# Kernel optimization log

Hardware: AMD Instinct MI355X
Metric: run time of the kernel (lower is better)

Reference implementation:

```python
import jax, jax.numpy as jnp
import numpy as np

DIM = 512
NT = 4      # n_tapes
HD = 64     # head_dim (mem_size)
SEQ = 1024
BATCH = 32
EPS = 1e-12


def _unitnorm(v, axis=-1):
    n = jnp.linalg.norm(v, axis=axis, keepdims=True)
    return v / jnp.maximum(n, EPS)


def setup_inputs() -> dict:
    key = jax.random.key(0)
    ks = jax.random.split(key, 16)
    s = 0.02
    p = lambda k, shape: jax.random.normal(k, shape, jnp.float32) * s
    return {
        "inputs": jax.random.normal(ks[0], (SEQ, BATCH, DIM), jnp.float32),
        "W_ih": p(ks[1], (4 * DIM, DIM)),
        "W_hh": p(ks[2], (4 * DIM, DIM)),
        "b_ih": p(ks[3], (4 * DIM,)),
        "b_hh": p(ks[4], (4 * DIM,)),
        "W_act": p(ks[5], (6 * NT, DIM)),
        "b_act": p(ks[6], (6 * NT,)),
        "W_val": p(ks[7], (HD * NT, DIM)),
        "b_val": p(ks[8], (HD * NT,)),
        "W_key": p(ks[9], (HD * NT, DIM)),
        "b_key": p(ks[10], (HD * NT,)),
        "W_q": p(ks[11], (HD * NT, DIM)),
        "b_q": p(ks[12], (HD * NT,)),
        "W_out": p(ks[13], (DIM, HD * NT)),
        "b_out": p(ks[14], (DIM,)),
        "tapelen": 64,
    }


def _lstm(inputs, W_ih, W_hh, b_ih, b_hh):
    # torch nn.LSTM, single layer, unidirectional, zero init state.
    S, B, D = inputs.shape
    gx = inputs @ W_ih.T + (b_ih + b_hh)  # [S,B,4D]

    def step(carry, g):
        h, c = carry
        g = g + h @ W_hh.T
        i, f, gg, o = jnp.split(g, 4, axis=-1)  # torch gate order i,f,g,o
        c = jax.nn.sigmoid(f) * c + jax.nn.sigmoid(i) * jnp.tanh(gg)
        h = jax.nn.sigmoid(o) * jnp.tanh(c)
        return (h, c), h

    h0 = jnp.zeros((B, D), inputs.dtype)
    (_, _), hs = jax.lax.scan(step, (h0, h0), gx)
    return hs  # [S,B,D]


def reference(inputs, W_ih, W_hh, b_ih, b_hh, W_act, b_act, W_val, b_val,
              W_key, b_key, W_q, b_q, W_out, b_out, tapelen):
    S, B, D = inputs.shape
    values = (inputs @ W_val.T + b_val).reshape(S, B, NT, HD)
    keys = _unitnorm((inputs @ W_key.T + b_key).reshape(S, B, NT, HD))

    hidden = _lstm(inputs, W_ih, W_hh, b_ih, b_hh)
    actions = (hidden @ W_act.T + b_act).reshape(S, B, NT, 6)
    dir_r = jax.nn.softmax(actions[..., 0:2], axis=-1)   # [S,B,NT,2]
    dir_w = jax.nn.softmax(actions[..., 2:4], axis=-1)
    rwprobs = jax.nn.sigmoid(actions[..., 4:6])
    queries = _unitnorm((hidden @ W_q.T + b_q).reshape(S, B, NT, HD))

    tape0 = jnp.zeros((tapelen, B, NT, HD), inputs.dtype)
    tkey0 = jnp.zeros_like(tape0)
    pos0 = jnp.zeros((tapelen, B, NT), inputs.dtype).at[0].set(1.0)

    def step(carry, xs):
        tape, tape_key, rpos, wpos = carry
        v, k, q, rd, wd, rw = xs
        wprob = rw[None, :, :, 1:2]                       # write gate
        oldval = jnp.einsum('lntc,lnt->ntc', tape, wpos)
        tape = tape + wpos[..., None] * (v - oldval)[None] * wprob
        read_out = jnp.einsum('lntc,lnt->ntc', tape, rpos)
        oldkey = jnp.einsum('lntc,lnt->ntc', tape_key, wpos)
        tape_key = tape_key + wpos[..., None] * (k - oldkey)[None] * wprob
        jpos = jnp.einsum('lntc,ntc->lnt', tape_key, q)
        jn = jnp.linalg.norm(jpos, axis=0, keepdims=True)  # normalize over tapelen
        jpos = jpos / jnp.maximum(jn, EPS)
        wpos_n = wpos * wd[None, :, :, 0] + jpos * wd[None, :, :, 1]
        out = read_out * rw[:, :, 0:1]                     # read gate
        rpos_n = rpos * rd[None, :, :, 0] + jpos * rd[None, :, :, 1]
        return (tape, tape_key, rpos_n, wpos_n), out

    (tape, _, _, _), read_outs = jax.lax.scan(
        step, (tape0, tkey0, pos0, pos0),
        (values, keys, queries, dir_r, dir_w, rwprobs))

    outputs = read_outs.reshape(S, B, NT * HD) @ W_out.T + b_out
    return outputs, tape.reshape(tapelen, B, HD * NT)
```

## Files before the change

### kernel.cpp

```cpp
#include <hip/hip_runtime.h>

typedef short short8 __attribute__((ext_vector_type(8)));
typedef float f32x4 __attribute__((ext_vector_type(4)));

__device__ __forceinline__ unsigned short f2bf(float x) {
  unsigned u = __builtin_bit_cast(unsigned, x);
  u += 0x7fffu + ((u >> 16) & 1u);
  return (unsigned short)(u >> 16);
}
__device__ __forceinline__ float bf2f(unsigned short v) {
  return __builtin_bit_cast(float, (unsigned)v << 16);
}
__device__ __forceinline__ float sigf(float x) { return 1.f / (1.f + __expf(-x)); }

__device__ __forceinline__ void split8(const float* __restrict__ vv, short8* h8, short8* l8) {
#pragma unroll
  for (int j = 0; j < 8; j++) {
    unsigned short hb = f2bf(vv[j]);
    unsigned short lb = f2bf(vv[j] - bf2f(hb));
    (*h8)[j] = (short)hb; (*l8)[j] = (short)lb;
  }
}
__device__ __forceinline__ void split_store8(const float* __restrict__ src,
                                             unsigned short* __restrict__ dhi,
                                             unsigned short* __restrict__ dlo) {
  float4 v0 = *(const float4*)src, v1 = *(const float4*)(src + 4);
  float vv[8] = {v0.x, v0.y, v0.z, v0.w, v1.x, v1.y, v1.z, v1.w};
  short8 h8, l8;
  split8(vv, &h8, &l8);
  *(short8*)dhi = h8; *(short8*)dlo = l8;
}

static constexpr size_t OFF_GX    = 0;
static constexpr size_t OFF_HC    = OFF_GX   + (size_t)4096*2048*4;
static constexpr size_t OFF_QUER  = OFF_HC   + (size_t)4096*512*4;
static constexpr size_t OFF_ACTS  = OFF_QUER + (size_t)32768*256*4;
static constexpr size_t OFF_R     = OFF_ACTS + (size_t)32768*24*4;
static constexpr size_t OFF_HB16  = OFF_R    + (size_t)32768*256*4;
static constexpr size_t OFF_CBUF  = OFF_HB16 + (size_t)2*2*32*512*2;
static constexpr size_t OFF_FLAGS = OFF_CBUF + (size_t)32*512*4;
static constexpr size_t WS_NEED   = OFF_FLAGS + 4096;

__global__ void zero_flags_kernel(unsigned int* flags) { flags[threadIdx.x] = 0u; }
__global__ void sentinel_kernel(float* p) { p[0] = 12345.0f; }

__global__ __launch_bounds__(256) void gemm_f32bt_kernel(
    const float* __restrict__ A, const float* __restrict__ Bw, float* __restrict__ C,
    const float* __restrict__ bias1, const float* __restrict__ bias2,
    int M, int N, int K) {
  const int bn = blockIdx.x, bm = blockIdx.y;
  const int tid = threadIdx.x;
  const int w = tid >> 6, l = tid & 63;
  const int wm = w >> 1, wn = w & 1;
  __shared__ __align__(16) unsigned short Ahs[128 * 40], Als[128 * 40];
  __shared__ __align__(16) unsigned short Bhs[128 * 40], Bls[128 * 40];
  f32x4 acc[4][4];
#pragma unroll
  for (int m = 0; m < 4; m++)
#pragma unroll
    for (int n = 0; n < 4; n++) acc[m][n] = (f32x4){0.f, 0.f, 0.f, 0.f};

  const int sr = tid >> 2;
  const int sk = (tid & 3) * 8;
  const size_t arow0 = (size_t)(bm * 128 + sr) * K;
  const size_t brow0 = (size_t)(bn * 128 + sr) * K;
  const int fr = l & 15, kb = (l >> 4) * 8;

  for (int kt = 0; kt < K; kt += 32) {
    __syncthreads();
    split_store8(A + arow0 + kt + sk,                  &Ahs[sr * 40 + sk],        &Als[sr * 40 + sk]);
    split_store8(A + arow0 + (size_t)64 * K + kt + sk, &Ahs[(sr + 64) * 40 + sk], &Als[(sr + 64) * 40 + sk]);
    split_store8(Bw + brow0 + kt + sk,                  &Bhs[sr * 40 + sk],        &Bls[sr * 40 + sk]);
    split_store8(Bw + brow0 + (size_t)64 * K + kt + sk, &Bhs[(sr + 64) * 40 + sk], &Bls[(sr + 64) * 40 + sk]);
    __syncthreads();
    short8 ah[4], al[4], bh[4], bl[4];
#pragma unroll
    for (int m = 0; m < 4; m++) {
      ah[m] = *(const short8*)&Ahs[(wm * 64 + m * 16 + fr) * 40 + kb];
      al[m] = *(const short8*)&Als[(wm * 64 + m * 16 + fr) * 40 + kb];
    }
#pragma unroll
    for (int n = 0; n < 4; n++) {
      bh[n] = *(const short8*)&Bhs[(wn * 64 + n * 16 + fr) * 40 + kb];
      bl[n] = *(const short8*)&Bls[(wn * 64 + n * 16 + fr) * 40 + kb];
    }
#pragma unroll
    for (int m = 0; m < 4; m++)
#pragma unroll
      for (int n = 0; n < 4; n++) {
        acc[m][n] = __builtin_amdgcn_mfma_f32_16x16x32_bf16(ah[m], bh[n], acc[m][n], 0, 0, 0);
        acc[m][n] = __builtin_amdgcn_mfma_f32_16x16x32_bf16(ah[m], bl[n], acc[m][n], 0, 0, 0);
        acc[m][n] = __builtin_amdgcn_mfma_f32_16x16x32_bf16(al[m], bh[n], acc[m][n], 0, 0, 0);
      }
  }
  const int cr = (l >> 4) * 4, cc = l & 15;
#pragma unroll
  for (int m = 0; m < 4; m++) {
#pragma unroll
    for (int n = 0; n < 4; n++) {
      int row0 = bm * 128 + wm * 64 + m * 16 + cr;
      int col = bn * 128 + wn * 64 + n * 16 + cc;
      float bv = bias1 ? bias1[col] : 0.f;
      if (bias2) bv += bias2[col];
#pragma unroll
      for (int r = 0; r < 4; r++) C[(size_t)(row0 + r) * N + col] = acc[m][n][r] + bv;
    }
  }
}

__global__ __launch_bounds__(256) void norm64_kernel(float* __restrict__ buf) {
  int g = blockIdx.x * 4 + (threadIdx.x >> 6);
  int lane = threadIdx.x & 63;
  float x = buf[(size_t)g * 64 + lane];
  float s = x * x;
#pragma unroll
  for (int m = 1; m < 64; m <<= 1) s += __shfl_xor(s, m, 64);
  buf[(size_t)g * 64 + lane] = x / fmaxf(sqrtf(s), 1e-12f);
}

__global__ __launch_bounds__(256) void lstm_kernel(const float* __restrict__ gxc,
                                                   const float* __restrict__ Whh,
                                                   unsigned short* __restrict__ hb16,
                                                   float* __restrict__ cbuf,
                                                   unsigned int* __restrict__ flags,
                                                   float* __restrict__ Hc,
                                                   int t0) {
  const int g = blockIdx.x;
  const int u0 = g * 8;
  const int tid = threadIdx.x;
  const int l = tid & 63, w = tid >> 6;
  __shared__ __align__(16) unsigned short Whi[32 * 512], Wlo[32 * 512];
  __shared__ __align__(16) unsigned short hhi[32 * 512], hlo[32 * 512];
  __shared__ float gates[32][33];

  {
    int r = tid >> 3, seg = tid & 7;
    int grow = (r >> 3) * 512 + u0 + (r & 7);
    const float* src = Whh + (size_t)grow * 512 + seg * 64;
#pragma unroll
    for (int i0 = 0; i0 < 64; i0 += 8) {
      int kg = seg * 8 + (i0 >> 3);
      int phys = r * 512 + ((kg ^ (r & 7)) << 3);
      split_store8(src + i0, &Whi[phys], &Wlo[phys]);
    }
  }
  if (t0 == 0) {
    for (int i = tid * 8; i < 32 * 512; i += 256 * 8) {
      short8 z = {0, 0, 0, 0, 0, 0, 0, 0};
      *(short8*)&hhi[i] = z; *(short8*)&hlo[i] = z;
    }
  }
  const int bb = tid >> 3, jj = tid & 7;
  float c = (t0 == 0) ? 0.f : cbuf[bb * 512 + u0 + jj];
  const int m = w >> 1, n = w & 1;
  const int arow = m * 16 + (l & 15), brow = n * 16 + (l & 15);
  const int asw = arow & 7, bsw = brow & 7;
  const int kq = l >> 4;
  __syncthreads();

  for (int t = t0; t < t0 + 128; ++t) {
    const float* gxr = gxc + ((size_t)(t - t0) * 32 + bb) * 2048;
    float xgi = gxr[u0 + jj];
    float xgf = gxr[512 + u0 + jj];
    float xgg = gxr[1024 + u0 + jj];
    float xgo = gxr[1536 + u0 + jj];
    if (t > 0) {
      if (tid < 64) {
        while (__hip_atomic_load(&flags[tid], __ATOMIC_RELAXED, __HIP_MEMORY_SCOPE_AGENT) < (unsigned)t)
          __builtin_amdgcn_s_sleep(1);
      }
      __syncthreads();
      const size_t pbase = (size_t)(t & 1) * 2 * 16384;
      const unsigned long long* hbh = (const unsigned long long*)(hb16 + pbase);
      const unsigned long long* hbl = (const unsigned long long*)(hb16 + pbase + 16384);
#pragma unroll
      for (int g8 = 0; g8 < 8; g8++) {
        int idx = g8 * 2048 + tid * 8;
        unsigned long long h0 = __hip_atomic_load(hbh + (idx >> 2),     __ATOMIC_RELAXED, __HIP_MEMORY_SCOPE_AGENT);
        unsigned long long h1 = __hip_atomic_load(hbh + (idx >> 2) + 1, __ATOMIC_RELAXED, __HIP_MEMORY_SCOPE_AGENT);
        unsigned long long l0 = __hip_atomic_load(hbl + (idx >> 2),     __ATOMIC_RELAXED, __HIP_MEMORY_SCOPE_AGENT);
        unsigned long long l1 = __hip_atomic_load(hbl + (idx >> 2) + 1, __ATOMIC_RELAXED, __HIP_MEMORY_SCOPE_AGENT);
        int b = idx >> 9, kg = (idx >> 3) & 63;
        int phys = b * 512 + ((kg ^ (b & 7)) << 3);
        *(unsigned long long*)&hhi[phys] = h0; *(unsigned long long*)&hhi[phys + 4] = h1;
        *(unsigned long long*)&hlo[phys] = l0; *(unsigned long long*)&hlo[phys + 4] = l1;
      }
      __syncthreads();
    }
    f32x4 acc = (f32x4){0.f, 0.f, 0.f, 0.f};
#pragma unroll
    for (int kt = 0; kt < 16; kt++) {
      int kg = kt * 4 + kq;
      short8 ah = *(const short8*)&hhi[arow * 512 + ((kg ^ asw) << 3)];
      short8 al = *(const short8*)&hlo[arow * 512 + ((kg ^ asw) << 3)];
      short8 bh = *(const short8*)&Whi[brow * 512 + ((kg ^ bsw) << 3)];
      short8 bl = *(const short8*)&Wlo[brow * 512 + ((kg ^ bsw) << 3)];
      acc = __builtin_amdgcn_mfma_f32_16x16x32_bf16(ah, bh, acc, 0, 0, 0);
      acc = __builtin_amdgcn_mfma_f32_16x16x32_bf16(ah, bl, acc, 0, 0, 0);
      acc = __builtin_amdgcn_mfma_f32_16x16x32_bf16(al, bh, acc, 0, 0, 0);
    }
    {
      int jcol = n * 16 + (l & 15), i0r = m * 16 + (l >> 4) * 4;
#pragma unroll
      for (int r = 0; r < 4; r++) gates[jcol][i0r + r] = acc[r];
    }
    __syncthreads();
    {
      float gi = gates[jj][bb]      + xgi;
      float gf = gates[8 + jj][bb]  + xgf;
      float gg = gates[16 + jj][bb] + xgg;
      float go = gates[24 + jj][bb] + xgo;
      c = sigf(gf) * c + sigf(gi) * tanhf(gg);
      float h = sigf(go) * tanhf(c);
      Hc[((size_t)(t - t0) * 32 + bb) * 512 + u0 + jj] = h;
      unsigned short hi16 = f2bf(h);
      unsigned short lo16 = f2bf(h - bf2f(hi16));
      const size_t pb2 = (size_t)((t + 1) & 1) * 2 * 16384;
      __hip_atomic_store(hb16 + pb2 + bb * 512 + u0 + jj, hi16,
                         __ATOMIC_RELAXED, __HIP_MEMORY_SCOPE_AGENT);
      __hip_atomic_store(hb16 + pb2 + 16384 + bb * 512 + u0 + jj, lo16,
                         __ATOMIC_RELAXED, __HIP_MEMORY_SCOPE_AGENT);
    }
    __syncthreads();
    if (tid == 0)
      __hip_atomic_store(&flags[g], (unsigned)(t + 1), __ATOMIC_RELAXED, __HIP_MEMORY_SCOPE_AGENT);
  }
  cbuf[bb * 512 + u0 + jj] = c;
}

__global__ __launch_bounds__(256) void actions_kernel(const float* __restrict__ H,
                                                      const float* __restrict__ Wact,
                                                      const float* __restrict__ bact,
                                                      float* __restrict__ acts) {
  const int wrow = threadIdx.x >> 6;
  const int row = blockIdx.x * 4 + wrow;
  const int lane = threadIdx.x & 63;
  __shared__ float a_s[4][24];
  const float* hp = H + (size_t)row * 512 + lane * 8;
  float4 h0 = *(const float4*)hp, h1 = *(const float4*)(hp + 4);
  float hf[8] = {h0.x, h0.y, h0.z, h0.w, h1.x, h1.y, h1.z, h1.w};
#pragma unroll
  for (int j = 0; j < 24; j++) {
    const float4* wr = (const float4*)(Wact + (size_t)j * 512 + lane * 8);
    float4 w0 = wr[0], w1 = wr[1];
    float p = hf[0] * w0.x + hf[1] * w0.y + hf[2] * w0.z + hf[3] * w0.w +
              hf[4] * w1.x + hf[5] * w1.y + hf[6] * w1.z + hf[7] * w1.w;
#pragma unroll
    for (int mm = 1; mm < 64; mm <<= 1) p += __shfl_xor(p, mm, 64);
    if (lane == j) a_s[wrow][j] = p + bact[j];
  }
  __syncthreads();
  if (lane < 4) {
    float av[6];
#pragma unroll
    for (int i = 0; i < 6; i++) av[i] = a_s[wrow][lane * 6 + i];
    float* o = acts + (size_t)row * 24 + lane * 6;
    o[0] = sigf(av[0] - av[1]); o[1] = sigf(av[1] - av[0]);
    o[2] = sigf(av[2] - av[3]); o[3] = sigf(av[3] - av[2]);
    o[4] = sigf(av[4]); o[5] = sigf(av[5]);
  }
}

__global__ __launch_bounds__(256) void tape_kernel(const float* __restrict__ vals,
                                                   const float* __restrict__ keys,
                                                   const float* __restrict__ quer,
                                                   const float* __restrict__ acts,
                                                   float* __restrict__ Rout,
                                                   float* __restrict__ out_tape) {
  const int bid = blockIdx.x;
  const int b = bid >> 2, nt = bid & 3;
  const int tid = threadIdx.x;
  const int cid = tid & 63, lg = tid >> 6;
  __shared__ float tape[64][65], tkey[64][65];
  __shared__ float redA[4][64], redB[4][64];
  __shared__ float wpos_s[64], rpos_s[64], q_s[64], dv_s[64], dk_s[64];
  for (int i = tid; i < 64 * 65; i += 256) { ((float*)tape)[i] = 0.f; ((float*)tkey)[i] = 0.f; }
  if (tid < 64) { wpos_s[tid] = (tid == 0) ? 1.f : 0.f; rpos_s[tid] = (tid == 0) ? 1.f : 0.f; }
  __syncthreads();

  float pv = 0.f, pk = 0.f, pq = 0.f;
  float2 pa0, pa1, pa2;
  {
    const size_t rc0 = ((size_t)b * 4 + nt) * 64;
    const float* a60 = acts + (size_t)b * 24 + nt * 6;
    if (tid < 64) { pv = vals[rc0 + tid]; pk = keys[rc0 + tid]; pq = quer[rc0 + tid]; }
    pa0 = *(const float2*)(a60); pa1 = *(const float2*)(a60 + 2); pa2 = *(const float2*)(a60 + 4);
  }

  for (int t = 0; t < 1024; ++t) {
    const float v = pv, k = pk, qv = pq;
    const float rd0 = pa0.x, rd1 = pa0.y, wd0 = pa1.x, wd1 = pa1.y, rw0 = pa2.x, rw1 = pa2.y;
    const size_t rc = (((size_t)t * 32 + b) * 4 + nt) * 64;
    if (tid < 64) q_s[tid] = qv;
    {
      int tn = (t + 1 < 1024) ? t + 1 : 1023;
      const size_t rbn = (size_t)tn * 32 + b;
      const size_t rcn = (rbn * 4 + nt) * 64;
      const float* a6n = acts + rbn * 24 + nt * 6;
      if (tid < 64) { pv = vals[rcn + tid]; pk = keys[rcn + tid]; pq = quer[rcn + tid]; }
      pa0 = *(const float2*)(a6n); pa1 = *(const float2*)(a6n + 2); pa2 = *(const float2*)(a6n + 4);
    }
    __syncthreads();
    float pa = 0.f, pb = 0.f;
#pragma unroll
    for (int i = 0; i < 16; i++) {
      int l2 = lg * 16 + i; float ww = wpos_s[l2];
      pa += tape[l2][cid] * ww; pb += tkey[l2][cid] * ww;
    }
    redA[lg][cid] = pa; redB[lg][cid] = pb;
    __syncthreads();
    if (tid < 64) {
      float ov = redA[0][cid] + redA[1][cid] + redA[2][cid] + redA[3][cid];
      float ok = redB[0][cid] + redB[1][cid] + redB[2][cid] + redB[3][cid];
      dv_s[cid] = (v - ov) * rw1;
      dk_s[cid] = (k - ok) * rw1;
    }
    __syncthreads();
    const float dv = dv_s[cid], dk = dk_s[cid];
    float pr = 0.f;
#pragma unroll
    for (int i = 0; i < 16; i++) {
      int l2 = lg * 16 + i; float ww = wpos_s[l2], r = rpos_s[l2];
      float tn2 = tape[l2][cid] + ww * dv; tape[l2][cid] = tn2; pr += tn2 * r;
      float kn = tkey[l2][cid] + ww * dk; tkey[l2][cid] = kn;
    }
    redA[lg][cid] = pr;
    __syncthreads();
    {
      const int lr = cid, cg = lg;
      float pj = 0.f;
#pragma unroll
      for (int i = 0; i < 16; i++) { int c2 = cg * 16 + i; pj += tkey[lr][c2] * q_s[c2]; }
      redB[cg][lr] = pj;
    }
    __syncthreads();
    if (tid < 64) {
      float jp = redB[0][tid] + redB[1][tid] + redB[2][tid] + redB[3][tid];
      float s = jp * jp;
#pragma unroll
      for (int mm = 1; mm < 64; mm <<= 1) s += __shfl_xor(s, mm, 64);
      jp /= fmaxf(sqrtf(s), 1e-12f);
      rpos_s[tid] = rpos_s[tid] * rd0 + jp * rd1;
      wpos_s[tid] = wpos_s[tid] * wd0 + jp * wd1;
    } else if (tid < 128) {
      int c2 = tid - 64;
      float ro = redA[0][c2] + redA[1][c2] + redA[2][c2] + redA[3][c2];
      Rout[rc + c2] = ro * rw0;
    }
  }
  __syncthreads();
  for (int i = tid; i < 4096; i += 256) {
    int l2 = i >> 6, c2 = i & 63;
    out_tape[((size_t)l2 * 32 + b) * 256 + nt * 64 + c2] = tape[l2][c2];
  }
}

extern "C" void kernel_launch(void* const* d_in, const int* in_sizes, int n_in,
                              void* d_out, int out_size, void* d_ws, size_t ws_size,
                              hipStream_t stream) {
  const float* inputs = (const float*)d_in[0];
  const float* W_ih = (const float*)d_in[1];
  const float* W_hh = (const float*)d_in[2];
  const float* b_ih = (const float*)d_in[3];
  const float* b_hh = (const float*)d_in[4];
  const float* W_act = (const float*)d_in[5];
  const float* b_act = (const float*)d_in[6];
  const float* W_val = (const float*)d_in[7];
  const float* b_val = (const float*)d_in[8];
  const float* W_key = (const float*)d_in[9];
  const float* b_key = (const float*)d_in[10];
  const float* W_q = (const float*)d_in[11];
  const float* b_q = (const float*)d_in[12];
  const float* W_out = (const float*)d_in[13];
  const float* b_out = (const float*)d_in[14];

  if (ws_size < WS_NEED) {
    sentinel_kernel<<<1, 1, 0, stream>>>((float*)d_out);
    return;
  }

  char* ws = (char*)d_ws;
  float* gxbuf = (float*)(ws + OFF_GX);
  float* Hc = (float*)(ws + OFF_HC);
  float* quer = (float*)(ws + OFF_QUER);
  float* acts = (float*)(ws + OFF_ACTS);
  float* R = (float*)(ws + OFF_R);
  unsigned short* hb16 = (unsigned short*)(ws + OFF_HB16);
  float* cbuf = (float*)(ws + OFF_CBUF);
  unsigned int* flags = (unsigned int*)(ws + OFF_FLAGS);

  float* keys = (float*)d_out;
  float* vals = (float*)d_out + 8388608;
  float* out_tape = (float*)d_out + 16777216;

  dim3 blk(256);
  zero_flags_kernel<<<1, 64, 0, stream>>>(flags);

  gemm_f32bt_kernel<<<dim3(2, 256), blk, 0, stream>>>(inputs, W_val, vals, b_val, nullptr, 32768, 256, 512);
  gemm_f32bt_kernel<<<dim3(2, 256), blk, 0, stream>>>(inputs, W_key, keys, b_key, nullptr, 32768, 256, 512);
  norm64_kernel<<<32768, blk, 0, stream>>>(keys);

  for (int q = 0; q < 8; q++) {
    const float* Achunk = inputs + (size_t)q * 4096 * 512;
    gemm_f32bt_kernel<<<dim3(16, 32), blk, 0, stream>>>(Achunk, W_ih, gxbuf, b_ih, b_hh, 4096, 2048, 512);
    lstm_kernel<<<64, blk, 0, stream>>>(gxbuf, W_hh, hb16, cbuf, flags, Hc, q * 128);
    gemm_f32bt_kernel<<<dim3(2, 32), blk, 0, stream>>>(Hc, W_q, quer + (size_t)q * 4096 * 256, b_q, nullptr, 4096, 256, 512);
    actions_kernel<<<1024, blk, 0, stream>>>(Hc, W_act, b_act, acts + (size_t)q * 4096 * 24);
  }
  norm64_kernel<<<32768, blk, 0, stream>>>(quer);

  tape_kernel<<<128, blk, 0, stream>>>(vals, keys, quer, acts, R, out_tape);

  gemm_f32bt_kernel<<<dim3(4, 256), blk, 0, stream>>>(R, W_out, (float*)d_out, b_out, nullptr, 32768, 512, 256);
}
```

Measured before the change: 7.878 ms.

## Use single-wave register-resident tape kernel and packed hi/lo LSTM hidden exchange

The tape recurrence kernel now runs one 64-thread wavefront per (batch, tape), keeping each column of the tape and the key tape in registers. All block barriers are dropped and only small LDS arrays are used for the position weights and the key-query products, which cuts per-step synchronisation on the 1024-step serial scan. The LSTM kernel packs the bf16 hi and lo halves of h into one 32-bit word, so each step needs one store per element and fewer, wider loads. Every wave now polls the flags with __all instead of one wave followed by a barrier. The costs are heavy register use (128 floats per thread) and more spinning across waves.

Result: slower. 12.51 ms (+58.8%).

```diff
diff --git a/kernel.cpp b/kernel.cpp
--- a/kernel.cpp
+++ b/kernel.cpp
@@ -36,8 +36,8 @@
 static constexpr size_t OFF_QUER  = OFF_HC   + (size_t)4096*512*4;
 static constexpr size_t OFF_ACTS  = OFF_QUER + (size_t)32768*256*4;
 static constexpr size_t OFF_R     = OFF_ACTS + (size_t)32768*24*4;
-static constexpr size_t OFF_HB16  = OFF_R    + (size_t)32768*256*4;
-static constexpr size_t OFF_CBUF  = OFF_HB16 + (size_t)2*2*32*512*2;
+static constexpr size_t OFF_HPK   = OFF_R    + (size_t)32768*256*4;
+static constexpr size_t OFF_CBUF  = OFF_HPK  + (size_t)2*32*512*4;
 static constexpr size_t OFF_FLAGS = OFF_CBUF + (size_t)32*512*4;
 static constexpr size_t WS_NEED   = OFF_FLAGS + 4096;
 
@@ -120,7 +120,7 @@
 
 __global__ __launch_bounds__(256) void lstm_kernel(const float* __restrict__ gxc,
                                                    const float* __restrict__ Whh,
-                                                   unsigned short* __restrict__ hb16,
+                                                   unsigned int* __restrict__ hpack,
                                                    float* __restrict__ cbuf,
                                                    unsigned int* __restrict__ flags,
                                                    float* __restrict__ Hc,
@@ -165,28 +165,34 @@
     float xgg = gxr[1024 + u0 + jj];
     float xgo = gxr[1536 + u0 + jj];
     if (t > 0) {
-      if (tid < 64) {
-        while (__hip_atomic_load(&flags[tid], __ATOMIC_RELAXED, __HIP_MEMORY_SCOPE_AGENT) < (unsigned)t)
-          __builtin_amdgcn_s_sleep(1);
+      for (;;) {
+        unsigned f = __hip_atomic_load(&flags[l], __ATOMIC_RELAXED, __HIP_MEMORY_SCOPE_AGENT);
+        if (__all((int)(f >= (unsigned)t))) break;
+        __builtin_amdgcn_s_sleep(2);
       }
-      __syncthreads();
-      const size_t pbase = (size_t)(t & 1) * 2 * 16384;
-      const unsigned long long* hbh = (const unsigned long long*)(hb16 + pbase);
-      const unsigned long long* hbl = (const unsigned long long*)(hb16 + pbase + 16384);
-#pragma unroll
-      for (int g8 = 0; g8 < 8; g8++) {
-        int idx = g8 * 2048 + tid * 8;
-        unsigned long long h0 = __hip_atomic_load(hbh + (idx >> 2),     __ATOMIC_RELAXED, __HIP_MEMORY_SCOPE_AGENT);
-        unsigned long long h1 = __hip_atomic_load(hbh + (idx >> 2) + 1, __ATOMIC_RELAXED, __HIP_MEMORY_SCOPE_AGENT);
-        unsigned long long l0 = __hip_atomic_load(hbl + (idx >> 2),     __ATOMIC_RELAXED, __HIP_MEMORY_SCOPE_AGENT);
-        unsigned long long l1 = __hip_atomic_load(hbl + (idx >> 2) + 1, __ATOMIC_RELAXED, __HIP_MEMORY_SCOPE_AGENT);
-        int b = idx >> 9, kg = (idx >> 3) & 63;
-        int phys = b * 512 + ((kg ^ (b & 7)) << 3);
-        *(unsigned long long*)&hhi[phys] = h0; *(unsigned long long*)&hhi[phys + 4] = h1;
-        *(unsigned long long*)&hlo[phys] = l0; *(unsigned long long*)&hlo[phys + 4] = l1;
+      const int b2 = tid >> 3, seg = tid & 7;
+      const unsigned long long* hq =
+          (const unsigned long long*)(hpack + (size_t)(t & 1) * 16384 + b2 * 512 + seg * 64);
+      unsigned long long lv[32];
+#pragma unroll
+      for (int i = 0; i < 32; i++)
+        lv[i] = __hip_atomic_load(hq + i, __ATOMIC_RELAXED, __HIP_MEMORY_SCOPE_AGENT);
+#pragma unroll
+      for (int gi = 0; gi < 8; gi++) {
+        short8 h8, l8;
+#pragma unroll
+        for (int p = 0; p < 4; p++) {
+          unsigned long long q2 = lv[gi * 4 + p];
+          unsigned v0 = (unsigned)q2, v1 = (unsigned)(q2 >> 32);
+          h8[2 * p]     = (short)(v0 & 0xffffu); l8[2 * p]     = (short)(v0 >> 16);
+          h8[2 * p + 1] = (short)(v1 & 0xffffu); l8[2 * p + 1] = (short)(v1 >> 16);
+        }
+        int kg = seg * 8 + gi;
+        int phys = b2 * 512 + ((kg ^ (b2 & 7)) << 3);
+        *(short8*)&hhi[phys] = h8; *(short8*)&hlo[phys] = l8;
       }
-      __syncthreads();
-    }
+    }
+    __syncthreads();
     f32x4 acc = (f32x4){0.f, 0.f, 0.f, 0.f};
 #pragma unroll
     for (int kt = 0; kt < 16; kt++) {
@@ -215,10 +221,8 @@
       Hc[((size_t)(t - t0) * 32 + bb) * 512 + u0 + jj] = h;
       unsigned short hi16 = f2bf(h);
       unsigned short lo16 = f2bf(h - bf2f(hi16));
-      const size_t pb2 = (size_t)((t + 1) & 1) * 2 * 16384;
-      __hip_atomic_store(hb16 + pb2 + bb * 512 + u0 + jj, hi16,
-                         __ATOMIC_RELAXED, __HIP_MEMORY_SCOPE_AGENT);
-      __hip_atomic_store(hb16 + pb2 + 16384 + bb * 512 + u0 + jj, lo16,
+      unsigned hv = (unsigned)hi16 | ((unsigned)lo16 << 16);
+      __hip_atomic_store(&hpack[(size_t)((t + 1) & 1) * 16384 + bb * 512 + u0 + jj], hv,
                          __ATOMIC_RELAXED, __HIP_MEMORY_SCOPE_AGENT);
     }
     __syncthreads();
@@ -261,98 +265,98 @@
   }
 }
 
-__global__ __launch_bounds__(256) void tape_kernel(const float* __restrict__ vals,
-                                                   const float* __restrict__ keys,
-                                                   const float* __restrict__ quer,
-                                                   const float* __restrict__ acts,
-                                                   float* __restrict__ Rout,
-                                                   float* __restrict__ out_tape) {
+__global__ __launch_bounds__(64) void tape_kernel(const float* __restrict__ vals,
+                                                  const float* __restrict__ keys,
+                                                  const float* __restrict__ quer,
+                                                  const float* __restrict__ acts,
+                                                  float* __restrict__ Rout,
+                                                  float* __restrict__ out_tape) {
   const int bid = blockIdx.x;
   const int b = bid >> 2, nt = bid & 3;
-  const int tid = threadIdx.x;
-  const int cid = tid & 63, lg = tid >> 6;
-  __shared__ float tape[64][65], tkey[64][65];
-  __shared__ float redA[4][64], redB[4][64];
-  __shared__ float wpos_s[64], rpos_s[64], q_s[64], dv_s[64], dk_s[64];
-  for (int i = tid; i < 64 * 65; i += 256) { ((float*)tape)[i] = 0.f; ((float*)tkey)[i] = 0.f; }
-  if (tid < 64) { wpos_s[tid] = (tid == 0) ? 1.f : 0.f; rpos_s[tid] = (tid == 0) ? 1.f : 0.f; }
-  __syncthreads();
-
-  float pv = 0.f, pk = 0.f, pq = 0.f;
+  const int c = threadIdx.x;
+  __shared__ float2 wr_lds[64];
+  __shared__ float prod[64][65];
+
+  float tape_r[64], tkey_r[64];
+#pragma unroll
+  for (int i = 0; i < 64; i++) { tape_r[i] = 0.f; tkey_r[i] = 0.f; }
+  float wown = (c == 0) ? 1.f : 0.f, rown = wown;
+  wr_lds[c] = make_float2(wown, rown);
+  asm volatile("" ::: "memory");
+
+  float pv, pk, pq;
   float2 pa0, pa1, pa2;
   {
     const size_t rc0 = ((size_t)b * 4 + nt) * 64;
     const float* a60 = acts + (size_t)b * 24 + nt * 6;
-    if (tid < 64) { pv = vals[rc0 + tid]; pk = keys[rc0 + tid]; pq = quer[rc0 + tid]; }
+    pv = vals[rc0 + c]; pk = keys[rc0 + c]; pq = quer[rc0 + c];
     pa0 = *(const float2*)(a60); pa1 = *(const float2*)(a60 + 2); pa2 = *(const float2*)(a60 + 4);
   }
 
   for (int t = 0; t < 1024; ++t) {
-    const float v = pv, k = pk, qv = pq;
+    const float v = pv, k = pk, q = pq;
     const float rd0 = pa0.x, rd1 = pa0.y, wd0 = pa1.x, wd1 = pa1.y, rw0 = pa2.x, rw1 = pa2.y;
     const size_t rc = (((size_t)t * 32 + b) * 4 + nt) * 64;
-    if (tid < 64) q_s[tid] = qv;
     {
       int tn = (t + 1 < 1024) ? t + 1 : 1023;
       const size_t rbn = (size_t)tn * 32 + b;
       const size_t rcn = (rbn * 4 + nt) * 64;
       const float* a6n = acts + rbn * 24 + nt * 6;
-      if (tid < 64) { pv = vals[rcn + tid]; pk = keys[rcn + tid]; pq = quer[rcn + tid]; }
+      pv = vals[rcn + c]; pk = keys[rcn + c]; pq = quer[rcn + c];
       pa0 = *(const float2*)(a6n); pa1 = *(const float2*)(a6n + 2); pa2 = *(const float2*)(a6n + 4);
     }
-    __syncthreads();
-    float pa = 0.f, pb = 0.f;
+    asm volatile("" ::: "memory");
+    float pa_0 = 0.f, pa_1 = 0.f, pa_2 = 0.f, pa_3 = 0.f;
+    float pb_0 = 0.f, pb_1 = 0.f, pb_2 = 0.f, pb_3 = 0.f;
 #pragma unroll
     for (int i = 0; i < 16; i++) {
-      int l2 = lg * 16 + i; float ww = wpos_s[l2];
-      pa += tape[l2][cid] * ww; pb += tkey[l2][cid] * ww;
-    }
-    redA[lg][cid] = pa; redB[lg][cid] = pb;
-    __syncthreads();
-    if (tid < 64) {
-      float ov = redA[0][cid] + redA[1][cid] + redA[2][cid] + redA[3][cid];
-      float ok = redB[0][cid] + redB[1][cid] + redB[2][cid] + redB[3][cid];
-      dv_s[cid] = (v - ov) * rw1;
-      dk_s[cid] = (k - ok) * rw1;
-    }
-    __syncthreads();
-    const float dv = dv_s[cid], dk = dk_s[cid];
-    float pr = 0.f;
+      float2 w0 = wr_lds[4 * i + 0], w1 = wr_lds[4 * i + 1];
+      float2 w2 = wr_lds[4 * i + 2], w3 = wr_lds[4 * i + 3];
+      pa_0 = fmaf(tape_r[4 * i + 0], w0.x, pa_0); pb_0 = fmaf(tkey_r[4 * i + 0], w0.x, pb_0);
+      pa_1 = fmaf(tape_r[4 * i + 1], w1.x, pa_1); pb_1 = fmaf(tkey_r[4 * i + 1], w1.x, pb_1);
+      pa_2 = fmaf(tape_r[4 * i + 2], w2.x, pa_2); pb_2 = fmaf(tkey_r[4 * i + 2], w2.x, pb_2);
+      pa_3 = fmaf(tape_r[4 * i + 3], w3.x, pa_3); pb_3 = fmaf(tkey_r[4 * i + 3], w3.x, pb_3);
+    }
+    const float dv = (v - ((pa_0 + pa_1) + (pa_2 + pa_3))) * rw1;
+    const float dk = (k - ((pb_0 + pb_1) + (pb_2 + pb_3))) * rw1;
+    float ro_0 = 0.f, ro_1 = 0.f, ro_2 = 0.f, ro_3 = 0.f;
 #pragma unroll
     for (int i = 0; i < 16; i++) {
-      int l2 = lg * 16 + i; float ww = wpos_s[l2], r = rpos_s[l2];
-      float tn2 = tape[l2][cid] + ww * dv; tape[l2][cid] = tn2; pr += tn2 * r;
-      float kn = tkey[l2][cid] + ww * dk; tkey[l2][cid] = kn;
-    }
-    redA[lg][cid] = pr;
-    __syncthreads();
-    {
-      const int lr = cid, cg = lg;
-      float pj = 0.f;
-#pragma unroll
-      for (int i = 0; i < 16; i++) { int c2 = cg * 16 + i; pj += tkey[lr][c2] * q_s[c2]; }
-      redB[cg][lr] = pj;
-    }
-    __syncthreads();
-    if (tid < 64) {
-      float jp = redB[0][tid] + redB[1][tid] + redB[2][tid] + redB[3][tid];
-      float s = jp * jp;
-#pragma unroll
-      for (int mm = 1; mm < 64; mm <<= 1) s += __shfl_xor(s, mm, 64);
-      jp /= fmaxf(sqrtf(s), 1e-12f);
-      rpos_s[tid] = rpos_s[tid] * rd0 + jp * rd1;
-      wpos_s[tid] = wpos_s[tid] * wd0 + jp * wd1;
-    } else if (tid < 128) {
-      int c2 = tid - 64;
-      float ro = redA[0][c2] + redA[1][c2] + redA[2][c2] + redA[3][c2];
-      Rout[rc + c2] = ro * rw0;
-    }
-  }
-  __syncthreads();
-  for (int i = tid; i < 4096; i += 256) {
-    int l2 = i >> 6, c2 = i & 63;
-    out_tape[((size_t)l2 * 32 + b) * 256 + nt * 64 + c2] = tape[l2][c2];
-  }
+      float2 w0 = wr_lds[4 * i + 0], w1 = wr_lds[4 * i + 1];
+      float2 w2 = wr_lds[4 * i + 2], w3 = wr_lds[4 * i + 3];
+      tape_r[4 * i + 0] = fmaf(w0.x, dv, tape_r[4 * i + 0]); ro_0 = fmaf(tape_r[4 * i + 0], w0.y, ro_0);
+      tape_r[4 * i + 1] = fmaf(w1.x, dv, tape_r[4 * i + 1]); ro_1 = fmaf(tape_r[4 * i + 1], w1.y, ro_1);
+      tape_r[4 * i + 2] = fmaf(w2.x, dv, tape_r[4 * i + 2]); ro_2 = fmaf(tape_r[4 * i + 2], w2.y, ro_2);
+      tape_r[4 * i + 3] = fmaf(w3.x, dv, tape_r[4 * i + 3]); ro_3 = fmaf(tape_r[4 * i + 3], w3.y, ro_3);
+      tkey_r[4 * i + 0] = fmaf(w0.x, dk, tkey_r[4 * i + 0]); prod[4 * i + 0][c] = tkey_r[4 * i + 0] * q;
+      tkey_r[4 * i + 1] = fmaf(w1.x, dk, tkey_r[4 * i + 1]); prod[4 * i + 1][c] = tkey_r[4 * i + 1] * q;
+      tkey_r[4 * i + 2] = fmaf(w2.x, dk, tkey_r[4 * i + 2]); prod[4 * i + 2][c] = tkey_r[4 * i + 2] * q;
+      tkey_r[4 * i + 3] = fmaf(w3.x, dk, tkey_r[4 * i + 3]); prod[4 * i + 3][c] = tkey_r[4 * i + 3] * q;
+    }
+    const float ro = (ro_0 + ro_1) + (ro_2 + ro_3);
+    asm volatile("" ::: "memory");
+    float jp_0 = 0.f, jp_1 = 0.f, jp_2 = 0.f, jp_3 = 0.f;
+#pragma unroll
+    for (int i = 0; i < 16; i++) {
+      jp_0 += prod[c][4 * i + 0];
+      jp_1 += prod[c][4 * i + 1];
+      jp_2 += prod[c][4 * i + 2];
+      jp_3 += prod[c][4 * i + 3];
+    }
+    float jp = (jp_0 + jp_1) + (jp_2 + jp_3);
+    float s = jp * jp;
+#pragma unroll
+    for (int mm = 1; mm < 64; mm <<= 1) s += __shfl_xor(s, mm, 64);
+    jp /= fmaxf(sqrtf(s), 1e-12f);
+    rown = rown * rd0 + jp * rd1;
+    wown = wown * wd0 + jp * wd1;
+    wr_lds[c] = make_float2(wown, rown);
+    Rout[rc + c] = ro * rw0;
+    asm volatile("" ::: "memory");
+  }
+#pragma unroll
+  for (int i = 0; i < 64; i++)
+    out_tape[((size_t)i * 32 + b) * 256 + nt * 64 + c] = tape_r[i];
 }
 
 extern "C" void kernel_launch(void* const* d_in, const int* in_sizes, int n_in,
@@ -385,7 +389,7 @@
   float* quer = (float*)(ws + OFF_QUER);
   float* acts = (float*)(ws + OFF_ACTS);
   float* R = (float*)(ws + OFF_R);
-  unsigned short* hb16 = (unsigned short*)(ws + OFF_HB16);
+  unsigned int* hpack = (unsigned int*)(ws + OFF_HPK);
   float* cbuf = (float*)(ws + OFF_CBUF);
   unsigned int* flags = (unsigned int*)(ws + OFF_FLAGS);
 
@@ -403,13 +407,13 @@
   for (int q = 0; q < 8; q++) {
     const float* Achunk = inputs + (size_t)q * 4096 * 512;
     gemm_f32bt_kernel<<<dim3(16, 32), blk, 0, stream>>>(Achunk, W_ih, gxbuf, b_ih, b_hh, 4096, 2048, 512);
-    lstm_kernel<<<64, blk, 0, stream>>>(gxbuf, W_hh, hb16, cbuf, flags, Hc, q * 128);
+    lstm_kernel<<<64, blk, 0, stream>>>(gxbuf, W_hh, hpack, cbuf, flags, Hc, q * 128);
     gemm_f32bt_kernel<<<dim3(2, 32), blk, 0, stream>>>(Hc, W_q, quer + (size_t)q * 4096 * 256, b_q, nullptr, 4096, 256, 512);
     actions_kernel<<<1024, blk, 0, stream>>>(Hc, W_act, b_act, acts + (size_t)q * 4096 * 24);
   }
   norm64_kernel<<<32768, blk, 0, stream>>>(quer);
 
-  tape_kernel<<<128, blk, 0, stream>>>(vals, keys, quer, acts, R, out_tape);
+  tape_kernel<<<128, 64, 0, stream>>>(vals, keys, quer, acts, R, out_tape);
 
   gemm_f32bt_kernel<<<dim3(4, 256), blk, 0, stream>>>(R, W_out, (float*)d_out, b_out, nullptr, 32768, 512, 256);
 }
```

## Pack LSTM hidden hi/lo into one word; restructure tape step with fewer barriers

Applied to the files above, without the earlier changes.

The LSTM exchange buffer now stores the bf16 hi and lo halves of each hidden value packed into one 32-bit word. Each step therefore does one atomic store per element, and readers unpack into the two LDS arrays. The tape scan is rewritten algebraically: the read-out and the key-query projection are computed from the pre-update tape and corrected by rank-1 terms. Position and query vectors are double-buffered, which cuts the per-step barriers from four to two. The aim is to shorten the serial per-step critical path of both recurrent kernels, at the cost of slightly different rounding order in the tape maths.

New measurement: 11.29 ms. +43.3%, slower.

```diff
diff --git a/kernel.cpp b/kernel.cpp
--- a/kernel.cpp
+++ b/kernel.cpp
@@ -36,8 +36,8 @@
 static constexpr size_t OFF_QUER  = OFF_HC   + (size_t)4096*512*4;
 static constexpr size_t OFF_ACTS  = OFF_QUER + (size_t)32768*256*4;
 static constexpr size_t OFF_R     = OFF_ACTS + (size_t)32768*24*4;
-static constexpr size_t OFF_HB16  = OFF_R    + (size_t)32768*256*4;
-static constexpr size_t OFF_CBUF  = OFF_HB16 + (size_t)2*2*32*512*2;
+static constexpr size_t OFF_HPK   = OFF_R    + (size_t)32768*256*4;
+static constexpr size_t OFF_CBUF  = OFF_HPK  + (size_t)2*32*512*4;
 static constexpr size_t OFF_FLAGS = OFF_CBUF + (size_t)32*512*4;
 static constexpr size_t WS_NEED   = OFF_FLAGS + 4096;
 
@@ -120,7 +120,7 @@
 
 __global__ __launch_bounds__(256) void lstm_kernel(const float* __restrict__ gxc,
                                                    const float* __restrict__ Whh,
-                                                   unsigned short* __restrict__ hb16,
+                                                   unsigned int* __restrict__ hpack,
                                                    float* __restrict__ cbuf,
                                                    unsigned int* __restrict__ flags,
                                                    float* __restrict__ Hc,
@@ -170,20 +170,29 @@
           __builtin_amdgcn_s_sleep(1);
       }
       __syncthreads();
-      const size_t pbase = (size_t)(t & 1) * 2 * 16384;
-      const unsigned long long* hbh = (const unsigned long long*)(hb16 + pbase);
-      const unsigned long long* hbl = (const unsigned long long*)(hb16 + pbase + 16384);
-#pragma unroll
-      for (int g8 = 0; g8 < 8; g8++) {
-        int idx = g8 * 2048 + tid * 8;
-        unsigned long long h0 = __hip_atomic_load(hbh + (idx >> 2),     __ATOMIC_RELAXED, __HIP_MEMORY_SCOPE_AGENT);
-        unsigned long long h1 = __hip_atomic_load(hbh + (idx >> 2) + 1, __ATOMIC_RELAXED, __HIP_MEMORY_SCOPE_AGENT);
-        unsigned long long l0 = __hip_atomic_load(hbl + (idx >> 2),     __ATOMIC_RELAXED, __HIP_MEMORY_SCOPE_AGENT);
-        unsigned long long l1 = __hip_atomic_load(hbl + (idx >> 2) + 1, __ATOMIC_RELAXED, __HIP_MEMORY_SCOPE_AGENT);
-        int b = idx >> 9, kg = (idx >> 3) & 63;
-        int phys = b * 512 + ((kg ^ (b & 7)) << 3);
-        *(unsigned long long*)&hhi[phys] = h0; *(unsigned long long*)&hhi[phys + 4] = h1;
-        *(unsigned long long*)&hlo[phys] = l0; *(unsigned long long*)&hlo[phys + 4] = l1;
+      const int b2 = tid >> 3, seg = tid & 7;
+      const unsigned long long* hq =
+          (const unsigned long long*)(hpack + (size_t)(t & 1) * 16384 + b2 * 512 + seg * 64);
+#pragma unroll
+      for (int grp = 0; grp < 2; grp++) {
+        unsigned long long lv[16];
+#pragma unroll
+        for (int i = 0; i < 16; i++)
+          lv[i] = __hip_atomic_load(hq + grp * 16 + i, __ATOMIC_RELAXED, __HIP_MEMORY_SCOPE_AGENT);
+#pragma unroll
+        for (int gi = 0; gi < 4; gi++) {
+          short8 h8, l8;
+#pragma unroll
+          for (int p = 0; p < 4; p++) {
+            unsigned long long q2 = lv[gi * 4 + p];
+            unsigned v0 = (unsigned)q2, v1 = (unsigned)(q2 >> 32);
+            h8[2 * p]     = (short)(v0 & 0xffffu); l8[2 * p]     = (short)(v0 >> 16);
+            h8[2 * p + 1] = (short)(v1 & 0xffffu); l8[2 * p + 1] = (short)(v1 >> 16);
+          }
+          int kg = seg * 8 + grp * 4 + gi;
+          int phys = b2 * 512 + ((kg ^ (b2 & 7)) << 3);
+          *(short8*)&hhi[phys] = h8; *(short8*)&hlo[phys] = l8;
+        }
       }
       __syncthreads();
     }
@@ -215,10 +224,8 @@
       Hc[((size_t)(t - t0) * 32 + bb) * 512 + u0 + jj] = h;
       unsigned short hi16 = f2bf(h);
       unsigned short lo16 = f2bf(h - bf2f(hi16));
-      const size_t pb2 = (size_t)((t + 1) & 1) * 2 * 16384;
-      __hip_atomic_store(hb16 + pb2 + bb * 512 + u0 + jj, hi16,
-                         __ATOMIC_RELAXED, __HIP_MEMORY_SCOPE_AGENT);
-      __hip_atomic_store(hb16 + pb2 + 16384 + bb * 512 + u0 + jj, lo16,
+      unsigned hv = (unsigned)hi16 | ((unsigned)lo16 << 16);
+      __hip_atomic_store(&hpack[(size_t)((t + 1) & 1) * 16384 + bb * 512 + u0 + jj], hv,
                          __ATOMIC_RELAXED, __HIP_MEMORY_SCOPE_AGENT);
     }
     __syncthreads();
@@ -272,11 +279,14 @@
   const int tid = threadIdx.x;
   const int cid = tid & 63, lg = tid >> 6;
   __shared__ float tape[64][65], tkey[64][65];
-  __shared__ float redA[4][64], redB[4][64];
-  __shared__ float wpos_s[64], rpos_s[64], q_s[64], dv_s[64], dk_s[64];
+  __shared__ float redA[4][64], redB[4][64], redC[4][64], redD[4][64];
+  __shared__ float dv_s[64], dk_s[64];
+  __shared__ float wpos_s[2][64], rpos_s[2][64], q_s[2][64];
   for (int i = tid; i < 64 * 65; i += 256) { ((float*)tape)[i] = 0.f; ((float*)tkey)[i] = 0.f; }
-  if (tid < 64) { wpos_s[tid] = (tid == 0) ? 1.f : 0.f; rpos_s[tid] = (tid == 0) ? 1.f : 0.f; }
-  __syncthreads();
+  if (tid < 64) {
+    wpos_s[0][tid] = (tid == 0) ? 1.f : 0.f;
+    rpos_s[0][tid] = (tid == 0) ? 1.f : 0.f;
+  }
 
   float pv = 0.f, pk = 0.f, pq = 0.f;
   float2 pa0, pa1, pa2;
@@ -286,12 +296,14 @@
     if (tid < 64) { pv = vals[rc0 + tid]; pk = keys[rc0 + tid]; pq = quer[rc0 + tid]; }
     pa0 = *(const float2*)(a60); pa1 = *(const float2*)(a60 + 2); pa2 = *(const float2*)(a60 + 4);
   }
+  if (tid < 64) q_s[0][tid] = pq;
+  __syncthreads();
 
   for (int t = 0; t < 1024; ++t) {
-    const float v = pv, k = pk, qv = pq;
+    const int p = t & 1;
+    const float v = pv, k = pk;
     const float rd0 = pa0.x, rd1 = pa0.y, wd0 = pa1.x, wd1 = pa1.y, rw0 = pa2.x, rw1 = pa2.y;
     const size_t rc = (((size_t)t * 32 + b) * 4 + nt) * 64;
-    if (tid < 64) q_s[tid] = qv;
     {
       int tn = (t + 1 < 1024) ? t + 1 : 1023;
       const size_t rbn = (size_t)tn * 32 + b;
@@ -300,14 +312,24 @@
       if (tid < 64) { pv = vals[rcn + tid]; pk = keys[rcn + tid]; pq = quer[rcn + tid]; }
       pa0 = *(const float2*)(a6n); pa1 = *(const float2*)(a6n + 2); pa2 = *(const float2*)(a6n + 4);
     }
-    __syncthreads();
-    float pa = 0.f, pb = 0.f;
-#pragma unroll
-    for (int i = 0; i < 16; i++) {
-      int l2 = lg * 16 + i; float ww = wpos_s[l2];
-      pa += tape[l2][cid] * ww; pb += tkey[l2][cid] * ww;
-    }
-    redA[lg][cid] = pa; redB[lg][cid] = pb;
+    {
+      float paA = 0.f, pbB = 0.f, prC = 0.f;
+#pragma unroll
+      for (int i = 0; i < 16; i++) {
+        int l2 = lg * 16 + i;
+        float tp = tape[l2][cid], tk = tkey[l2][cid];
+        float wp = wpos_s[p][l2], rp = rpos_s[p][l2];
+        paA = fmaf(tp, wp, paA); pbB = fmaf(tk, wp, pbB); prC = fmaf(tp, rp, prC);
+      }
+      redA[lg][cid] = paA; redB[lg][cid] = pbB; redC[lg][cid] = prC;
+      float pj = 0.f;
+#pragma unroll
+      for (int i = 0; i < 16; i++) {
+        int c2 = lg * 16 + i;
+        pj = fmaf(tkey[cid][c2], q_s[p][c2], pj);
+      }
+      redD[lg][cid] = pj;
+    }
     __syncthreads();
     if (tid < 64) {
       float ov = redA[0][cid] + redA[1][cid] + redA[2][cid] + redA[3][cid];
@@ -316,39 +338,36 @@
       dk_s[cid] = (k - ok) * rw1;
     }
     __syncthreads();
-    const float dv = dv_s[cid], dk = dk_s[cid];
-    float pr = 0.f;
+    const float dvc = dv_s[cid], dkc = dk_s[cid];
 #pragma unroll
     for (int i = 0; i < 16; i++) {
-      int l2 = lg * 16 + i; float ww = wpos_s[l2], r = rpos_s[l2];
-      float tn2 = tape[l2][cid] + ww * dv; tape[l2][cid] = tn2; pr += tn2 * r;
-      float kn = tkey[l2][cid] + ww * dk; tkey[l2][cid] = kn;
-    }
-    redA[lg][cid] = pr;
-    __syncthreads();
-    {
-      const int lr = cid, cg = lg;
-      float pj = 0.f;
-#pragma unroll
-      for (int i = 0; i < 16; i++) { int c2 = cg * 16 + i; pj += tkey[lr][c2] * q_s[c2]; }
-      redB[cg][lr] = pj;
-    }
-    __syncthreads();
-    if (tid < 64) {
-      float jp = redB[0][tid] + redB[1][tid] + redB[2][tid] + redB[3][tid];
+      int l2 = lg * 16 + i;
+      float wp = wpos_s[p][l2];
+      tape[l2][cid] = fmaf(wp, dvc, tape[l2][cid]);
+      tkey[l2][cid] = fmaf(wp, dkc, tkey[l2][cid]);
+    }
+    if (lg == 0) {
+      float prc = redC[0][cid] + redC[1][cid] + redC[2][cid] + redC[3][cid];
+      float sw = wpos_s[p][cid] * rpos_s[p][cid];
+#pragma unroll
+      for (int mm = 1; mm < 64; mm <<= 1) sw += __shfl_xor(sw, mm, 64);
+      Rout[rc + cid] = (prc + sw * dvc) * rw0;
+      q_s[p ^ 1][cid] = pq;
+    } else if (lg == 1) {
+      float jq = redD[0][cid] + redD[1][cid] + redD[2][cid] + redD[3][cid];
+      float dq = dk_s[cid] * q_s[p][cid];
+#pragma unroll
+      for (int mm = 1; mm < 64; mm <<= 1) dq += __shfl_xor(dq, mm, 64);
+      float jp = fmaf(wpos_s[p][cid], dq, jq);
       float s = jp * jp;
 #pragma unroll
       for (int mm = 1; mm < 64; mm <<= 1) s += __shfl_xor(s, mm, 64);
       jp /= fmaxf(sqrtf(s), 1e-12f);
-      rpos_s[tid] = rpos_s[tid] * rd0 + jp * rd1;
-      wpos_s[tid] = wpos_s[tid] * wd0 + jp * wd1;
-    } else if (tid < 128) {
-      int c2 = tid - 64;
-      float ro = redA[0][c2] + redA[1][c2] + redA[2][c2] + redA[3][c2];
-      Rout[rc + c2] = ro * rw0;
-    }
-  }
-  __syncthreads();
+      rpos_s[p ^ 1][cid] = rpos_s[p][cid] * rd0 + jp * rd1;
+      wpos_s[p ^ 1][cid] = wpos_s[p][cid] * wd0 + jp * wd1;
+    }
+    __syncthreads();
+  }
   for (int i = tid; i < 4096; i += 256) {
     int l2 = i >> 6, c2 = i & 63;
     out_tape[((size_t)l2 * 32 + b) * 256 + nt * 64 + c2] = tape[l2][c2];
@@ -385,7 +404,7 @@
   float* quer = (float*)(ws + OFF_QUER);
   float* acts = (float*)(ws + OFF_ACTS);
   float* R = (float*)(ws + OFF_R);
-  unsigned short* hb16 = (unsigned short*)(ws + OFF_HB16);
+  unsigned int* hpack = (unsigned int*)(ws + OFF_HPK);
   float* cbuf = (float*)(ws + OFF_CBUF);
   unsigned int* flags = (unsigned int*)(ws + OFF_FLAGS);
 
@@ -403,7 +422,7 @@
   for (int q = 0; q < 8; q++) {
     const float* Achunk = inputs + (size_t)q * 4096 * 512;
     gemm_f32bt_kernel<<<dim3(16, 32), blk, 0, stream>>>(Achunk, W_ih, gxbuf, b_ih, b_hh, 4096, 2048, 512);
-    lstm_kernel<<<64, blk, 0, stream>>>(gxbuf, W_hh, hb16, cbuf, flags, Hc, q * 128);
+    lstm_kernel<<<64, blk, 0, stream>>>(gxbuf, W_hh, hpack, cbuf, flags, Hc, q * 128);
     gemm_f32bt_kernel<<<dim3(2, 32), blk, 0, stream>>>(Hc, W_q, quer + (size_t)q * 4096 * 256, b_q, nullptr, 4096, 256, 512);
     actions_kernel<<<1024, blk, 0, stream>>>(Hc, W_act, b_act, acts + (size_t)q * 4096 * 24);
   }
```

## Restructure tape recurrence to fuse reductions and cut barriers with 1024 threads

Applied to the files above, without the earlier changes.

The tape step kernel now runs with 1024 threads per block and computes the write-position, read-position and query dot products from the old tape in a single pass. It recovers the post-update read output and jpos algebraically through rank-one correction terms (sum of w*r times dv, and sum of dk*q times w), which removes the dependent passes over the updated tape. Position and query buffers are double-buffered so each step needs three barriers instead of five. The risks are extra reductions over 16 partials and small floating-point reordering differences.

Measured after the change: 7.715 ms (median of 4 runs). 1.02x faster.

```diff
diff --git a/kernel.cpp b/kernel.cpp
--- a/kernel.cpp
+++ b/kernel.cpp
@@ -261,22 +261,25 @@
   }
 }
 
-__global__ __launch_bounds__(256) void tape_kernel(const float* __restrict__ vals,
-                                                   const float* __restrict__ keys,
-                                                   const float* __restrict__ quer,
-                                                   const float* __restrict__ acts,
-                                                   float* __restrict__ Rout,
-                                                   float* __restrict__ out_tape) {
+__global__ __launch_bounds__(1024) void tape_kernel(const float* __restrict__ vals,
+                                                    const float* __restrict__ keys,
+                                                    const float* __restrict__ quer,
+                                                    const float* __restrict__ acts,
+                                                    float* __restrict__ Rout,
+                                                    float* __restrict__ out_tape) {
   const int bid = blockIdx.x;
   const int b = bid >> 2, nt = bid & 3;
   const int tid = threadIdx.x;
   const int cid = tid & 63, lg = tid >> 6;
   __shared__ float tape[64][65], tkey[64][65];
-  __shared__ float redA[4][64], redB[4][64];
-  __shared__ float wpos_s[64], rpos_s[64], q_s[64], dv_s[64], dk_s[64];
-  for (int i = tid; i < 64 * 65; i += 256) { ((float*)tape)[i] = 0.f; ((float*)tkey)[i] = 0.f; }
-  if (tid < 64) { wpos_s[tid] = (tid == 0) ? 1.f : 0.f; rpos_s[tid] = (tid == 0) ? 1.f : 0.f; }
-  __syncthreads();
+  __shared__ float redA[16][64], redB[16][64], redC[16][64], redD[16][64];
+  __shared__ float dv_s[64], dk_s[64];
+  __shared__ float wpos_s[2][64], rpos_s[2][64], q_s[2][64];
+  for (int i = tid; i < 64 * 65; i += 1024) { ((float*)tape)[i] = 0.f; ((float*)tkey)[i] = 0.f; }
+  if (tid < 64) {
+    wpos_s[0][tid] = (tid == 0) ? 1.f : 0.f;
+    rpos_s[0][tid] = (tid == 0) ? 1.f : 0.f;
+  }
 
   float pv = 0.f, pk = 0.f, pq = 0.f;
   float2 pa0, pa1, pa2;
@@ -286,12 +289,14 @@
     if (tid < 64) { pv = vals[rc0 + tid]; pk = keys[rc0 + tid]; pq = quer[rc0 + tid]; }
     pa0 = *(const float2*)(a60); pa1 = *(const float2*)(a60 + 2); pa2 = *(const float2*)(a60 + 4);
   }
+  if (tid < 64) q_s[0][tid] = pq;
+  __syncthreads();
 
   for (int t = 0; t < 1024; ++t) {
-    const float v = pv, k = pk, qv = pq;
+    const int p = t & 1;
+    const float v = pv, k = pk;
     const float rd0 = pa0.x, rd1 = pa0.y, wd0 = pa1.x, wd1 = pa1.y, rw0 = pa2.x, rw1 = pa2.y;
     const size_t rc = (((size_t)t * 32 + b) * 4 + nt) * 64;
-    if (tid < 64) q_s[tid] = qv;
     {
       int tn = (t + 1 < 1024) ? t + 1 : 1023;
       const size_t rbn = (size_t)tn * 32 + b;
@@ -300,56 +305,64 @@
       if (tid < 64) { pv = vals[rcn + tid]; pk = keys[rcn + tid]; pq = quer[rcn + tid]; }
       pa0 = *(const float2*)(a6n); pa1 = *(const float2*)(a6n + 2); pa2 = *(const float2*)(a6n + 4);
     }
-    __syncthreads();
-    float pa = 0.f, pb = 0.f;
-#pragma unroll
-    for (int i = 0; i < 16; i++) {
-      int l2 = lg * 16 + i; float ww = wpos_s[l2];
-      pa += tape[l2][cid] * ww; pb += tkey[l2][cid] * ww;
-    }
-    redA[lg][cid] = pa; redB[lg][cid] = pb;
-    __syncthreads();
-    if (tid < 64) {
-      float ov = redA[0][cid] + redA[1][cid] + redA[2][cid] + redA[3][cid];
-      float ok = redB[0][cid] + redB[1][cid] + redB[2][cid] + redB[3][cid];
+    {
+      float paA = 0.f, pbB = 0.f, prC = 0.f, pj = 0.f;
+#pragma unroll
+      for (int i = 0; i < 4; i++) {
+        int l2 = lg * 4 + i;
+        float tp = tape[l2][cid], tk = tkey[l2][cid];
+        float wp = wpos_s[p][l2], rp = rpos_s[p][l2];
+        paA = fmaf(tp, wp, paA); pbB = fmaf(tk, wp, pbB); prC = fmaf(tp, rp, prC);
+        int c2 = lg * 4 + i;
+        pj = fmaf(tkey[cid][c2], q_s[p][c2], pj);
+      }
+      redA[lg][cid] = paA; redB[lg][cid] = pbB; redC[lg][cid] = prC; redD[lg][cid] = pj;
+    }
+    __syncthreads();
+    if (lg == 0) {
+      float ov = 0.f, ok = 0.f;
+#pragma unroll
+      for (int j = 0; j < 16; j++) { ov += redA[j][cid]; ok += redB[j][cid]; }
       dv_s[cid] = (v - ov) * rw1;
       dk_s[cid] = (k - ok) * rw1;
     }
     __syncthreads();
-    const float dv = dv_s[cid], dk = dk_s[cid];
-    float pr = 0.f;
-#pragma unroll
-    for (int i = 0; i < 16; i++) {
-      int l2 = lg * 16 + i; float ww = wpos_s[l2], r = rpos_s[l2];
-      float tn2 = tape[l2][cid] + ww * dv; tape[l2][cid] = tn2; pr += tn2 * r;
-      float kn = tkey[l2][cid] + ww * dk; tkey[l2][cid] = kn;
-    }
-    redA[lg][cid] = pr;
-    __syncthreads();
-    {
-      const int lr = cid, cg = lg;
-      float pj = 0.f;
-#pragma unroll
-      for (int i = 0; i < 16; i++) { int c2 = cg * 16 + i; pj += tkey[lr][c2] * q_s[c2]; }
-      redB[cg][lr] = pj;
-    }
-    __syncthreads();
-    if (tid < 64) {
-      float jp = redB[0][tid] + redB[1][tid] + redB[2][tid] + redB[3][tid];
+    const float dvc = dv_s[cid], dkc = dk_s[cid];
+#pragma unroll
+    for (int i = 0; i < 4; i++) {
+      int l2 = lg * 4 + i;
+      float wp = wpos_s[p][l2];
+      tape[l2][cid] = fmaf(wp, dvc, tape[l2][cid]);
+      tkey[l2][cid] = fmaf(wp, dkc, tkey[l2][cid]);
+    }
+    if (lg == 0) {
+      q_s[p ^ 1][cid] = pq;
+    } else if (lg == 1) {
+      float prc = 0.f;
+#pragma unroll
+      for (int j = 0; j < 16; j++) prc += redC[j][cid];
+      float sw = wpos_s[p][cid] * rpos_s[p][cid];
+#pragma unroll
+      for (int mm = 1; mm < 64; mm <<= 1) sw += __shfl_xor(sw, mm, 64);
+      Rout[rc + cid] = fmaf(sw, dvc, prc) * rw0;
+    } else if (lg == 2) {
+      float jq = 0.f;
+#pragma unroll
+      for (int j = 0; j < 16; j++) jq += redD[j][cid];
+      float dq = dkc * q_s[p][cid];
+#pragma unroll
+      for (int mm = 1; mm < 64; mm <<= 1) dq += __shfl_xor(dq, mm, 64);
+      float jp = fmaf(wpos_s[p][cid], dq, jq);
       float s = jp * jp;
 #pragma unroll
       for (int mm = 1; mm < 64; mm <<= 1) s += __shfl_xor(s, mm, 64);
       jp /= fmaxf(sqrtf(s), 1e-12f);
-      rpos_s[tid] = rpos_s[tid] * rd0 + jp * rd1;
-      wpos_s[tid] = wpos_s[tid] * wd0 + jp * wd1;
-    } else if (tid < 128) {
-      int c2 = tid - 64;
-      float ro = redA[0][c2] + redA[1][c2] + redA[2][c2] + redA[3][c2];
-      Rout[rc + c2] = ro * rw0;
-    }
-  }
-  __syncthreads();
-  for (int i = tid; i < 4096; i += 256) {
+      rpos_s[p ^ 1][cid] = rpos_s[p][cid] * rd0 + jp * rd1;
+      wpos_s[p ^ 1][cid] = wpos_s[p][cid] * wd0 + jp * wd1;
+    }
+    __syncthreads();
+  }
+  for (int i = tid; i < 4096; i += 1024) {
     int l2 = i >> 6, c2 = i & 63;
     out_tape[((size_t)l2 * 32 + b) * 256 + nt * 64 + c2] = tape[l2][c2];
   }
@@ -409,7 +422,7 @@
   }
   norm64_kernel<<<32768, blk, 0, stream>>>(quer);
 
-  tape_kernel<<<128, blk, 0, stream>>>(vals, keys, quer, acts, R, out_tape);
+  tape_kernel<<<128, 1024, 0, stream>>>(vals, keys, quer, acts, R, out_tape);
 
   gemm_f32bt_kernel<<<dim3(4, 256), blk, 0, stream>>>(R, W_out, (float*)d_out, b_out, nullptr, 32768, 512, 256);
 }
```
